# Kernel tuning notes

Hardware: AMD Instinct MI355X
Metric: run time of the kernel (lower is better)

## Reference

```python
import jax, jax.numpy as jnp
import numpy as np

N, F, E, LIN, C, B = 16384, 500, 128, 128, 10, 4096
P_EDGE = 0.002  # ~32 avg degree


def _l2norm(x):
    # F.normalize(dim=1), eps=1e-12
    n = jnp.linalg.norm(x, axis=1, keepdims=True)
    return x / jnp.maximum(n, 1e-12)


def setup_inputs() -> dict:
    key = jax.random.key(0)
    ks = jax.random.split(key, 10)
    adj = (jax.random.uniform(ks[0], (N, N)) < P_EDGE).astype(jnp.float32)
    idx = jnp.arange(N)
    adj = adj.at[idx, idx].set(1.0)  # self-loops guarantee degree >= 1
    data = jax.random.normal(ks[1], (N, F), dtype=jnp.float32)
    nodes = jax.random.randint(ks[2], (B,), 0, N)
    # Encoder 1: Linear(2F -> E); Encoder 2: Linear(2E -> E); classifier heads
    W1 = jax.random.normal(ks[3], (E, 2 * F), dtype=jnp.float32) * 0.03
    b1 = jnp.zeros((E,), jnp.float32)
    W2 = jax.random.normal(ks[4], (E, 2 * E), dtype=jnp.float32) * 0.06
    b2 = jnp.zeros((E,), jnp.float32)
    Wl1 = jax.random.normal(ks[5], (LIN, E), dtype=jnp.float32) * 0.08
    bl1 = jnp.zeros((LIN,), jnp.float32)
    Wl2 = jax.random.normal(ks[6], (C, LIN), dtype=jnp.float32) * 0.12
    bl2 = jnp.zeros((C,), jnp.float32)
    return {"nodes": nodes, "adj": adj, "data": data,
            "W1": W1, "b1": b1, "W2": W2, "b2": b2,
            "Wl1": Wl1, "bl1": bl1, "Wl2": Wl2, "bl2": bl2}


def reference(nodes, adj, data, W1, b1, W2, b2, Wl1, bl1, Wl2, bl2):
    deg = jnp.sum(adj, axis=1, keepdims=True)  # [N,1]
    # Layer 1 (mean aggregator over full neighbor set): computed for all nodes
    neigh1 = (adj @ data) / deg                               # [N,F]
    h1 = jnp.concatenate([data, neigh1], axis=1)              # [N,2F] (self, neigh)
    H1 = _l2norm(jax.nn.relu(h1 @ W1.T + b1))                 # [N,E]
    # Layer 2: only for the queried node batch
    neigh2 = (adj[nodes] @ H1) / deg[nodes]                   # [B,E]
    h2 = jnp.concatenate([H1[nodes], neigh2], axis=1)         # [B,2E]
    H2 = _l2norm(jax.nn.relu(h2 @ W2.T + b2))                 # [B,E]
    x = H2 @ Wl1.T + bl1                                      # [B,LIN]
    x = x @ Wl2.T + bl2                                       # [B,C]
    return jax.nn.softmax(x, axis=1)
```

## Files before the change

### kernel.cpp

```cpp
#include <hip/hip_runtime.h>
#include <math.h>
#include <stddef.h>

#define N_NODES 16384
#define F_DIM   500
#define KP1     512
#define E_DIM   128
#define C_DIM   10
#define B_DIM   4096
#define MAXDEG  128

typedef __attribute__((ext_vector_type(8))) short short8;
typedef __attribute__((ext_vector_type(4))) float f32x4;

__device__ inline unsigned short f2bf(float f) {
    union { float f; unsigned int u; } v; v.f = f;
    unsigned int u = v.u;
    u += 0x7FFFu + ((u >> 16) & 1u);
    return (unsigned short)(u >> 16);
}

__global__ __launch_bounds__(256) void k_prep_w1b(const float* __restrict__ W1,
                                                  unsigned short* __restrict__ Wt) {
    int idx = blockIdx.x * 256 + threadIdx.x;
    int n = idx >> 9, k = idx & 511;
    float v = (k < F_DIM) ? W1[(size_t)(n & 127) * 1000 + (n >> 7) * F_DIM + k] : 0.0f;
    Wt[idx] = f2bf(v);
}

__global__ __launch_bounds__(256) void k_prep_w2b(const float* __restrict__ W2,
                                                  unsigned short* __restrict__ Wt) {
    int idx = blockIdx.x * 256 + threadIdx.x;
    int n = idx >> 7, k = idx & 127;
    Wt[idx] = f2bf(W2[(size_t)(n & 127) * 256 + (n >> 7) * 128 + k]);
}

__global__ void k_tp(const float* __restrict__ src, float* __restrict__ dst) {
    __shared__ float tile[32][33];
    const int k0 = blockIdx.x * 32;
    const int e0 = blockIdx.y * 32;
    const int tx = threadIdx.x, ty0 = threadIdx.y;
#pragma unroll
    for (int q = 0; q < 4; ++q) {
        int ty = ty0 + q * 8;
        tile[ty][tx] = src[(size_t)(e0 + ty) * 128 + k0 + tx];
    }
    __syncthreads();
#pragma unroll
    for (int q = 0; q < 4; ++q) {
        int ty = ty0 + q * 8;
        dst[(size_t)(k0 + ty) * 128 + e0 + tx] = tile[tx][ty];
    }
}

__global__ __launch_bounds__(256) void k_gemm_mfma(const void* __restrict__ Ap,
                                                   int Ka, int Kpad, int a_fp32,
                                                   const unsigned short* __restrict__ B,
                                                   float* __restrict__ Cout) {
    __shared__ unsigned short sA[32 * 40];
    __shared__ unsigned short sB[256 * 40];
    const int tid  = threadIdx.x;
    const int w    = tid >> 6;
    const int lane = tid & 63;
    const int l16  = lane & 15;
    const int quad = lane >> 4;
    const int blockM = blockIdx.x * 32;
    f32x4 acc[2][4] = {};
    const int nchunks = Kpad >> 5;

    for (int c = 0; c < nchunks; ++c) {
        const int k0 = c << 5;
        if (tid < 128) {
            int row = tid >> 2, cc = tid & 3;
            int kbase = k0 + cc * 8;
            short8 v;
            if (a_fp32) {
                const float* Arow = (const float*)Ap + (size_t)(blockM + row) * Ka;
                float4 f0 = (kbase + 4 <= Ka) ? *(const float4*)(Arow + kbase)
                                              : make_float4(0.f, 0.f, 0.f, 0.f);
                float4 f1 = (kbase + 8 <= Ka) ? *(const float4*)(Arow + kbase + 4)
                                              : make_float4(0.f, 0.f, 0.f, 0.f);
                v[0] = (short)f2bf(f0.x); v[1] = (short)f2bf(f0.y);
                v[2] = (short)f2bf(f0.z); v[3] = (short)f2bf(f0.w);
                v[4] = (short)f2bf(f1.x); v[5] = (short)f2bf(f1.y);
                v[6] = (short)f2bf(f1.z); v[7] = (short)f2bf(f1.w);
            } else {
                v = *(const short8*)((const unsigned short*)Ap +
                                     (size_t)(blockM + row) * Ka + kbase);
            }
            *(short8*)(sA + row * 40 + cc * 8) = v;
        }
#pragma unroll
        for (int q = 0; q < 4; ++q) {
            int idx = tid + 256 * q;
            int row = idx >> 2, cc = idx & 3;
            short8 v = *(const short8*)(B + (size_t)row * Kpad + k0 + cc * 8);
            *(short8*)(sB + row * 40 + cc * 8) = v;
        }
        __syncthreads();
        short8 af[2], bf[4];
#pragma unroll
        for (int mt = 0; mt < 2; ++mt)
            af[mt] = *(const short8*)(sA + (mt * 16 + l16) * 40 + quad * 8);
#pragma unroll
        for (int nt = 0; nt < 4; ++nt)
            bf[nt] = *(const short8*)(sB + (w * 64 + nt * 16 + l16) * 40 + quad * 8);
#pragma unroll
        for (int mt = 0; mt < 2; ++mt)
#pragma unroll
            for (int nt = 0; nt < 4; ++nt)
                acc[mt][nt] = __builtin_amdgcn_mfma_f32_16x16x32_bf16(af[mt], bf[nt], acc[mt][nt], 0, 0, 0);
        __syncthreads();
    }
#pragma unroll
    for (int mt = 0; mt < 2; ++mt)
#pragma unroll
        for (int nt = 0; nt < 4; ++nt) {
            int col = w * 64 + nt * 16 + l16;
#pragma unroll
            for (int r = 0; r < 4; ++r) {
                int row = blockM + mt * 16 + quad * 4 + r;
                Cout[(size_t)row * 256 + col] = acc[mt][nt][r];
            }
        }
}

__global__ __launch_bounds__(256) void k_agg1(const float* __restrict__ adj,
                                              const float* __restrict__ X,
                                              const float* __restrict__ b1,
                                              unsigned short* __restrict__ H1b,
                                              int* __restrict__ nbr,
                                              int* __restrict__ deg) {
    const int i = blockIdx.x;
    const int t = threadIdx.x;
    const float4* row4 = (const float4*)(adj + (size_t)i * N_NODES);
    __shared__ int s_cnt;
    __shared__ int s_idx[MAXDEG];
    __shared__ float s_part[8][128];
    __shared__ float s_w[2];
    if (t == 0) s_cnt = 0;
    __syncthreads();
    float4 v[16];
#pragma unroll
    for (int p = 0; p < 16; ++p) v[p] = row4[p * 256 + t];
#pragma unroll
    for (int p = 0; p < 16; ++p) {
        int col = p * 1024 + t * 4;
        if (v[p].x != 0.f) { int q = atomicAdd(&s_cnt, 1); if (q < MAXDEG) s_idx[q] = col;     }
        if (v[p].y != 0.f) { int q = atomicAdd(&s_cnt, 1); if (q < MAXDEG) s_idx[q] = col + 1; }
        if (v[p].z != 0.f) { int q = atomicAdd(&s_cnt, 1); if (q < MAXDEG) s_idx[q] = col + 2; }
        if (v[p].w != 0.f) { int q = atomicAdd(&s_cnt, 1); if (q < MAXDEG) s_idx[q] = col + 3; }
    }
    __syncthreads();
    int cnt = s_cnt; if (cnt > MAXDEG) cnt = MAXDEG;
    if (t < cnt) nbr[(size_t)i * MAXDEG + t] = s_idx[t];
    if (t == 0) deg[i] = cnt;
    const float inv = 1.0f / (float)cnt;
    const int g = t >> 5, l = t & 31;
    float4 a4 = make_float4(0.f, 0.f, 0.f, 0.f);
    for (int k = g; k < cnt; k += 8) {
        float4 x4 = ((const float4*)(X + (size_t)s_idx[k] * 256 + 128))[l];
        a4.x += x4.x; a4.y += x4.y; a4.z += x4.z; a4.w += x4.w;
    }
    *(float4*)&s_part[g][l * 4] = a4;
    __syncthreads();
    float vv = 0.f;
    if (t < 128) {
        float tot = 0.f;
#pragma unroll
        for (int g2 = 0; g2 < 8; ++g2) tot += s_part[g2][t];
        vv = X[(size_t)i * 256 + t] + tot * inv + b1[t];
        vv = fmaxf(vv, 0.f);
        float s = vv * vv;
#pragma unroll
        for (int off = 32; off > 0; off >>= 1) s += __shfl_down(s, off, 64);
        if ((t & 63) == 0) s_w[t >> 6] = s;
    }
    __syncthreads();
    if (t < 128) {
        float denom = fmaxf(sqrtf(s_w[0] + s_w[1]), 1e-12f);
        H1b[(size_t)i * 128 + t] = f2bf(vv / denom);
    }
}

__global__ __launch_bounds__(256) void k_l2head(const int* __restrict__ nodes,
                                                const int* __restrict__ nbr,
                                                const int* __restrict__ deg,
                                                const float* __restrict__ Y,
                                                const float* __restrict__ b2,
                                                const float* __restrict__ Wl1t,
                                                const float* __restrict__ bl1,
                                                const float* __restrict__ Wl2,
                                                const float* __restrict__ bl2,
                                                float* __restrict__ out) {
    const int b = blockIdx.x;
    const int t = threadIdx.x;
    const int n = nodes[b];
    const int cnt = deg[n];
    __shared__ int s_idx[MAXDEG];
    __shared__ float s_part[8][128];
    __shared__ float s_h[128];
    __shared__ float s_x[128];
    __shared__ float s_c[C_DIM];
    __shared__ float s_w[2];
    if (t < cnt) s_idx[t] = nbr[(size_t)n * MAXDEG + t];
    __syncthreads();
    const int g = t >> 5, l = t & 31;
    float4 a4 = make_float4(0.f, 0.f, 0.f, 0.f);
    for (int k = g; k < cnt; k += 8) {
        float4 y4 = ((const float4*)(Y + (size_t)s_idx[k] * 256 + 128))[l];
        a4.x += y4.x; a4.y += y4.y; a4.z += y4.z; a4.w += y4.w;
    }
    *(float4*)&s_part[g][l * 4] = a4;
    __syncthreads();
    if (t < 128) {
        float tot = 0.f;
#pragma unroll
        for (int g2 = 0; g2 < 8; ++g2) tot += s_part[g2][t];
        float vv = Y[(size_t)n * 256 + t] + tot / (float)cnt + b2[t];
        vv = fmaxf(vv, 0.f);
        float s = vv * vv;
#pragma unroll
        for (int off = 32; off > 0; off >>= 1) s += __shfl_down(s, off, 64);
        if ((t & 63) == 0) s_w[t >> 6] = s;
        __syncthreads();
        float denom = fmaxf(sqrtf(s_w[0] + s_w[1]), 1e-12f);
        s_h[t] = vv / denom;
    } else {
        __syncthreads();
    }
    __syncthreads();
    if (t < 128) {
        float x1 = bl1[t];
#pragma unroll 8
        for (int kk = 0; kk < 128; ++kk)
            x1 += Wl1t[kk * 128 + t] * s_h[kk];
        s_x[t] = x1;
    }
    __syncthreads();
    if (t < C_DIM) {
        float l2 = bl2[t];
        const float* wr = Wl2 + (size_t)t * 128;
        for (int kk = 0; kk < 128; ++kk) l2 += wr[kk] * s_x[kk];
        s_c[t] = l2;
    }
    __syncthreads();
    if (t < C_DIM) {
        float mx = -1e30f;
        for (int c = 0; c < C_DIM; ++c) mx = fmaxf(mx, s_c[c]);
        float se = 0.f;
        for (int c = 0; c < C_DIM; ++c) se += expf(s_c[c] - mx);
        out[(size_t)b * C_DIM + t] = expf(s_c[t] - mx) / se;
    }
}

extern "C" void kernel_launch(void* const* d_in, const int* in_sizes, int n_in,
                              void* d_out, int out_size, void* d_ws, size_t ws_size,
                              hipStream_t stream) {
    const int*   nodes = (const int*)  d_in[0];
    const float* adj   = (const float*)d_in[1];
    const float* data  = (const float*)d_in[2];
    const float* W1    = (const float*)d_in[3];
    const float* b1    = (const float*)d_in[4];
    const float* W2    = (const float*)d_in[5];
    const float* b2    = (const float*)d_in[6];
    const float* Wl1   = (const float*)d_in[7];
    const float* bl1   = (const float*)d_in[8];
    const float* Wl2   = (const float*)d_in[9];
    const float* bl2   = (const float*)d_in[10];
    float* out = (float*)d_out;

    unsigned short* Wt1 = (unsigned short*)d_ws;
    unsigned short* Wt2 = Wt1 + 256 * KP1;
    unsigned short* H1b = Wt2 + 256 * 128;
    float* Wl1t = (float*)(H1b + (size_t)N_NODES * 128);
    float* X    = Wl1t + 128 * 128;
    float* Y    = X    + (size_t)N_NODES * 256;
    int*   nbr  = (int*)(Y + (size_t)N_NODES * 256);
    int*   deg  = nbr + (size_t)N_NODES * MAXDEG;

    k_prep_w1b <<<512, 256, 0, stream>>>(W1, Wt1);
    k_prep_w2b <<<128, 256, 0, stream>>>(W2, Wt2);
    k_tp<<<dim3(4, 4), dim3(32, 8), 0, stream>>>(Wl1, Wl1t);

    k_gemm_mfma<<<N_NODES / 32, 256, 0, stream>>>(data, F_DIM, KP1, 1, Wt1, X);
    k_agg1     <<<N_NODES, 256, 0, stream>>>(adj, X, b1, H1b, nbr, deg);

    k_gemm_mfma<<<N_NODES / 32, 256, 0, stream>>>(H1b, E_DIM, E_DIM, 0, Wt2, Y);
    k_l2head   <<<B_DIM, 256, 0, stream>>>(nodes, nbr, deg, Y, b2, Wl1t, bl1, Wl2, bl2, out);
}
```

Baseline: 1.424 ms.

## Overlap layer-1 GEMM with adjacency scan in one mixed kernel, split gather

```diff
diff --git a/kernel.cpp b/kernel.cpp
--- a/kernel.cpp
+++ b/kernel.cpp
@@ -20,41 +20,179 @@
     return (unsigned short)(u >> 16);
 }
 
-__global__ __launch_bounds__(256) void k_prep_w1b(const float* __restrict__ W1,
-                                                  unsigned short* __restrict__ Wt) {
-    int idx = blockIdx.x * 256 + threadIdx.x;
-    int n = idx >> 9, k = idx & 511;
-    float v = (k < F_DIM) ? W1[(size_t)(n & 127) * 1000 + (n >> 7) * F_DIM + k] : 0.0f;
-    Wt[idx] = f2bf(v);
-}
-
-__global__ __launch_bounds__(256) void k_prep_w2b(const float* __restrict__ W2,
-                                                  unsigned short* __restrict__ Wt) {
-    int idx = blockIdx.x * 256 + threadIdx.x;
-    int n = idx >> 7, k = idx & 127;
-    Wt[idx] = f2bf(W2[(size_t)(n & 127) * 256 + (n >> 7) * 128 + k]);
-}
-
-__global__ void k_tp(const float* __restrict__ src, float* __restrict__ dst) {
-    __shared__ float tile[32][33];
-    const int k0 = blockIdx.x * 32;
-    const int e0 = blockIdx.y * 32;
-    const int tx = threadIdx.x, ty0 = threadIdx.y;
-#pragma unroll
-    for (int q = 0; q < 4; ++q) {
-        int ty = ty0 + q * 8;
-        tile[ty][tx] = src[(size_t)(e0 + ty) * 128 + k0 + tx];
-    }
-    __syncthreads();
-#pragma unroll
-    for (int q = 0; q < 4; ++q) {
-        int ty = ty0 + q * 8;
-        dst[(size_t)(k0 + ty) * 128 + e0 + tx] = tile[tx][ty];
-    }
-}
-
-__global__ __launch_bounds__(256) void k_gemm_mfma(const void* __restrict__ Ap,
-                                                   int Ka, int Kpad, int a_fp32,
+__global__ __launch_bounds__(256) void k_prep(const float* __restrict__ W1,
+                                              const float* __restrict__ W2,
+                                              const float* __restrict__ Wl1,
+                                              unsigned short* __restrict__ Wt1,
+                                              unsigned short* __restrict__ Wt2,
+                                              float* __restrict__ Wl1t) {
+    const int bb = blockIdx.x;
+    const int t = threadIdx.x;
+    if (bb < 512) {
+        int idx = bb * 256 + t;
+        int n = idx >> 9, k = idx & 511;
+        float v = (k < F_DIM) ? W1[(size_t)(n & 127) * 1000 + (n >> 7) * F_DIM + k] : 0.0f;
+        Wt1[idx] = f2bf(v);
+    } else if (bb < 640) {
+        int idx = (bb - 512) * 256 + t;
+        int n = idx >> 7, k = idx & 127;
+        Wt2[idx] = f2bf(W2[(size_t)(n & 127) * 256 + (n >> 7) * 128 + k]);
+    } else {
+        __shared__ float tile[32][33];
+        int tb = bb - 640;
+        int k0 = (tb & 3) * 32, e0 = (tb >> 2) * 32;
+        int tx = t & 31, ty0 = t >> 5;
+#pragma unroll
+        for (int q = 0; q < 4; ++q) {
+            int ty = ty0 + q * 8;
+            tile[ty][tx] = Wl1[(size_t)(e0 + ty) * 128 + k0 + tx];
+        }
+        __syncthreads();
+#pragma unroll
+        for (int q = 0; q < 4; ++q) {
+            int ty = ty0 + q * 8;
+            Wl1t[(size_t)(k0 + ty) * 128 + e0 + tx] = tile[tx][ty];
+        }
+    }
+}
+
+__global__ __launch_bounds__(256) void k_mix(const float* __restrict__ data,
+                                             const unsigned short* __restrict__ Wt1,
+                                             float* __restrict__ X,
+                                             const float* __restrict__ adj,
+                                             unsigned short* __restrict__ nbr,
+                                             int* __restrict__ deg) {
+    __shared__ alignas(16) unsigned char s_raw[(32 * 40 + 256 * 40) * 2];
+    const int bb = blockIdx.x;
+    const int tid = threadIdx.x;
+
+    if (bb < 512) {
+        unsigned short* sA = (unsigned short*)s_raw;
+        unsigned short* sB = sA + 32 * 40;
+        const int w    = tid >> 6;
+        const int lane = tid & 63;
+        const int l16  = lane & 15;
+        const int quad = lane >> 4;
+        const int blockM = bb * 32;
+        f32x4 acc[2][4] = {};
+#pragma unroll 1
+        for (int c = 0; c < (KP1 >> 5); ++c) {
+            const int k0 = c << 5;
+            if (tid < 128) {
+                int row = tid >> 2, cc = tid & 3;
+                int kbase = k0 + cc * 8;
+                const float* Arow = data + (size_t)(blockM + row) * F_DIM;
+                float4 f0 = (kbase + 4 <= F_DIM) ? *(const float4*)(Arow + kbase)
+                                                 : make_float4(0.f, 0.f, 0.f, 0.f);
+                float4 f1 = (kbase + 8 <= F_DIM) ? *(const float4*)(Arow + kbase + 4)
+                                                 : make_float4(0.f, 0.f, 0.f, 0.f);
+                short8 v;
+                v[0] = (short)f2bf(f0.x); v[1] = (short)f2bf(f0.y);
+                v[2] = (short)f2bf(f0.z); v[3] = (short)f2bf(f0.w);
+                v[4] = (short)f2bf(f1.x); v[5] = (short)f2bf(f1.y);
+                v[6] = (short)f2bf(f1.z); v[7] = (short)f2bf(f1.w);
+                *(short8*)(sA + row * 40 + cc * 8) = v;
+            }
+#pragma unroll
+            for (int q = 0; q < 4; ++q) {
+                int idx = tid + 256 * q;
+                int row = idx >> 2, cc = idx & 3;
+                short8 v = *(const short8*)(Wt1 + (size_t)row * KP1 + k0 + cc * 8);
+                *(short8*)(sB + row * 40 + cc * 8) = v;
+            }
+            __syncthreads();
+            short8 af[2], bf[4];
+#pragma unroll
+            for (int mt = 0; mt < 2; ++mt)
+                af[mt] = *(const short8*)(sA + (mt * 16 + l16) * 40 + quad * 8);
+#pragma unroll
+            for (int nt = 0; nt < 4; ++nt)
+                bf[nt] = *(const short8*)(sB + (w * 64 + nt * 16 + l16) * 40 + quad * 8);
+#pragma unroll
+            for (int mt = 0; mt < 2; ++mt)
+#pragma unroll
+                for (int nt = 0; nt < 4; ++nt)
+                    acc[mt][nt] = __builtin_amdgcn_mfma_f32_16x16x32_bf16(af[mt], bf[nt], acc[mt][nt], 0, 0, 0);
+            __syncthreads();
+        }
+#pragma unroll
+        for (int mt = 0; mt < 2; ++mt)
+#pragma unroll
+            for (int nt = 0; nt < 4; ++nt) {
+                int col = w * 64 + nt * 16 + l16;
+#pragma unroll
+                for (int r = 0; r < 4; ++r) {
+                    int row = blockM + mt * 16 + quad * 4 + r;
+                    X[(size_t)row * 256 + col] = acc[mt][nt][r];
+                }
+            }
+    } else {
+        const int i = bb - 512;
+        int* s_cnt = (int*)s_raw;
+        int* s_idx = ((int*)s_raw) + 4;
+        const float4* row4 = (const float4*)(adj + (size_t)i * N_NODES);
+        if (tid == 0) *s_cnt = 0;
+        __syncthreads();
+        float4 v[16];
+#pragma unroll
+        for (int p = 0; p < 16; ++p) v[p] = row4[p * 256 + tid];
+#pragma unroll
+        for (int p = 0; p < 16; ++p) {
+            int col = p * 1024 + tid * 4;
+            if (v[p].x != 0.f) { int q = atomicAdd(s_cnt, 1); if (q < MAXDEG) s_idx[q] = col;     }
+            if (v[p].y != 0.f) { int q = atomicAdd(s_cnt, 1); if (q < MAXDEG) s_idx[q] = col + 1; }
+            if (v[p].z != 0.f) { int q = atomicAdd(s_cnt, 1); if (q < MAXDEG) s_idx[q] = col + 2; }
+            if (v[p].w != 0.f) { int q = atomicAdd(s_cnt, 1); if (q < MAXDEG) s_idx[q] = col + 3; }
+        }
+        __syncthreads();
+        int cnt = *s_cnt; if (cnt > MAXDEG) cnt = MAXDEG;
+        if (tid < cnt) nbr[(size_t)i * MAXDEG + tid] = (unsigned short)s_idx[tid];
+        if (tid == 0) deg[i] = cnt;
+    }
+}
+
+__global__ __launch_bounds__(256) void k_gather(const unsigned short* __restrict__ nbr,
+                                                const int* __restrict__ deg,
+                                                const float* __restrict__ X,
+                                                const float* __restrict__ b1,
+                                                unsigned short* __restrict__ H1b) {
+    const int i = blockIdx.x;
+    const int t = threadIdx.x;
+    const int cnt = deg[i];
+    __shared__ int s_idx[MAXDEG];
+    __shared__ float s_part[8][128];
+    __shared__ float s_w[2];
+    if (t < cnt) s_idx[t] = nbr[(size_t)i * MAXDEG + t];
+    __syncthreads();
+    const int g = t >> 5, l = t & 31;
+    float4 a4 = make_float4(0.f, 0.f, 0.f, 0.f);
+    for (int k = g; k < cnt; k += 8) {
+        float4 x4 = ((const float4*)(X + (size_t)s_idx[k] * 256 + 128))[l];
+        a4.x += x4.x; a4.y += x4.y; a4.z += x4.z; a4.w += x4.w;
+    }
+    *(float4*)&s_part[g][l * 4] = a4;
+    __syncthreads();
+    float vv = 0.f;
+    if (t < 128) {
+        float tot = 0.f;
+#pragma unroll
+        for (int g2 = 0; g2 < 8; ++g2) tot += s_part[g2][t];
+        vv = X[(size_t)i * 256 + t] + tot / (float)cnt + b1[t];
+        vv = fmaxf(vv, 0.f);
+        float s = vv * vv;
+#pragma unroll
+        for (int off = 32; off > 0; off >>= 1) s += __shfl_down(s, off, 64);
+        if ((t & 63) == 0) s_w[t >> 6] = s;
+    }
+    __syncthreads();
+    if (t < 128) {
+        float denom = fmaxf(sqrtf(s_w[0] + s_w[1]), 1e-12f);
+        H1b[(size_t)i * 128 + t] = f2bf(vv / denom);
+    }
+}
+
+__global__ __launch_bounds__(256) void k_gemm_mfma(const unsigned short* __restrict__ A,
+                                                   int K,
                                                    const unsigned short* __restrict__ B,
                                                    float* __restrict__ Cout) {
     __shared__ unsigned short sA[32 * 40];
@@ -66,35 +204,18 @@
     const int quad = lane >> 4;
     const int blockM = blockIdx.x * 32;
     f32x4 acc[2][4] = {};
-    const int nchunks = Kpad >> 5;
-
-    for (int c = 0; c < nchunks; ++c) {
+    for (int c = 0; c < (K >> 5); ++c) {
         const int k0 = c << 5;
         if (tid < 128) {
             int row = tid >> 2, cc = tid & 3;
-            int kbase = k0 + cc * 8;
-            short8 v;
-            if (a_fp32) {
-                const float* Arow = (const float*)Ap + (size_t)(blockM + row) * Ka;
-                float4 f0 = (kbase + 4 <= Ka) ? *(const float4*)(Arow + kbase)
-                                              : make_float4(0.f, 0.f, 0.f, 0.f);
-                float4 f1 = (kbase + 8 <= Ka) ? *(const float4*)(Arow + kbase + 4)
-                                              : make_float4(0.f, 0.f, 0.f, 0.f);
-                v[0] = (short)f2bf(f0.x); v[1] = (short)f2bf(f0.y);
-                v[2] = (short)f2bf(f0.z); v[3] = (short)f2bf(f0.w);
-                v[4] = (short)f2bf(f1.x); v[5] = (short)f2bf(f1.y);
-                v[6] = (short)f2bf(f1.z); v[7] = (short)f2bf(f1.w);
-            } else {
-                v = *(const short8*)((const unsigned short*)Ap +
-                                     (size_t)(blockM + row) * Ka + kbase);
-            }
+            short8 v = *(const short8*)(A + (size_t)(blockM + row) * K + k0 + cc * 8);
             *(short8*)(sA + row * 40 + cc * 8) = v;
         }
 #pragma unroll
         for (int q = 0; q < 4; ++q) {
             int idx = tid + 256 * q;
             int row = idx >> 2, cc = idx & 3;
-            short8 v = *(const short8*)(B + (size_t)row * Kpad + k0 + cc * 8);
+            short8 v = *(const short8*)(B + (size_t)row * K + k0 + cc * 8);
             *(short8*)(sB + row * 40 + cc * 8) = v;
         }
         __syncthreads();
@@ -125,66 +246,8 @@
         }
 }
 
-__global__ __launch_bounds__(256) void k_agg1(const float* __restrict__ adj,
-                                              const float* __restrict__ X,
-                                              const float* __restrict__ b1,
-                                              unsigned short* __restrict__ H1b,
-                                              int* __restrict__ nbr,
-                                              int* __restrict__ deg) {
-    const int i = blockIdx.x;
-    const int t = threadIdx.x;
-    const float4* row4 = (const float4*)(adj + (size_t)i * N_NODES);
-    __shared__ int s_cnt;
-    __shared__ int s_idx[MAXDEG];
-    __shared__ float s_part[8][128];
-    __shared__ float s_w[2];
-    if (t == 0) s_cnt = 0;
-    __syncthreads();
-    float4 v[16];
-#pragma unroll
-    for (int p = 0; p < 16; ++p) v[p] = row4[p * 256 + t];
-#pragma unroll
-    for (int p = 0; p < 16; ++p) {
-        int col = p * 1024 + t * 4;
-        if (v[p].x != 0.f) { int q = atomicAdd(&s_cnt, 1); if (q < MAXDEG) s_idx[q] = col;     }
-        if (v[p].y != 0.f) { int q = atomicAdd(&s_cnt, 1); if (q < MAXDEG) s_idx[q] = col + 1; }
-        if (v[p].z != 0.f) { int q = atomicAdd(&s_cnt, 1); if (q < MAXDEG) s_idx[q] = col + 2; }
-        if (v[p].w != 0.f) { int q = atomicAdd(&s_cnt, 1); if (q < MAXDEG) s_idx[q] = col + 3; }
-    }
-    __syncthreads();
-    int cnt = s_cnt; if (cnt > MAXDEG) cnt = MAXDEG;
-    if (t < cnt) nbr[(size_t)i * MAXDEG + t] = s_idx[t];
-    if (t == 0) deg[i] = cnt;
-    const float inv = 1.0f / (float)cnt;
-    const int g = t >> 5, l = t & 31;
-    float4 a4 = make_float4(0.f, 0.f, 0.f, 0.f);
-    for (int k = g; k < cnt; k += 8) {
-        float4 x4 = ((const float4*)(X + (size_t)s_idx[k] * 256 + 128))[l];
-        a4.x += x4.x; a4.y += x4.y; a4.z += x4.z; a4.w += x4.w;
-    }
-    *(float4*)&s_part[g][l * 4] = a4;
-    __syncthreads();
-    float vv = 0.f;
-    if (t < 128) {
-        float tot = 0.f;
-#pragma unroll
-        for (int g2 = 0; g2 < 8; ++g2) tot += s_part[g2][t];
-        vv = X[(size_t)i * 256 + t] + tot * inv + b1[t];
-        vv = fmaxf(vv, 0.f);
-        float s = vv * vv;
-#pragma unroll
-        for (int off = 32; off > 0; off >>= 1) s += __shfl_down(s, off, 64);
-        if ((t & 63) == 0) s_w[t >> 6] = s;
-    }
-    __syncthreads();
-    if (t < 128) {
-        float denom = fmaxf(sqrtf(s_w[0] + s_w[1]), 1e-12f);
-        H1b[(size_t)i * 128 + t] = f2bf(vv / denom);
-    }
-}
-
 __global__ __launch_bounds__(256) void k_l2head(const int* __restrict__ nodes,
-                                                const int* __restrict__ nbr,
+                                                const unsigned short* __restrict__ nbr,
                                                 const int* __restrict__ deg,
                                                 const float* __restrict__ Y,
                                                 const float* __restrict__ b2,
@@ -276,16 +339,14 @@
     float* Wl1t = (float*)(H1b + (size_t)N_NODES * 128);
     float* X    = Wl1t + 128 * 128;
     float* Y    = X    + (size_t)N_NODES * 256;
-    int*   nbr  = (int*)(Y + (size_t)N_NODES * 256);
-    int*   deg  = nbr + (size_t)N_NODES * MAXDEG;
-
-    k_prep_w1b <<<512, 256, 0, stream>>>(W1, Wt1);
-    k_prep_w2b <<<128, 256, 0, stream>>>(W2, Wt2);
-    k_tp<<<dim3(4, 4), dim3(32, 8), 0, stream>>>(Wl1, Wl1t);
-
-    k_gemm_mfma<<<N_NODES / 32, 256, 0, stream>>>(data, F_DIM, KP1, 1, Wt1, X);
-    k_agg1     <<<N_NODES, 256, 0, stream>>>(adj, X, b1, H1b, nbr, deg);
-
-    k_gemm_mfma<<<N_NODES / 32, 256, 0, stream>>>(H1b, E_DIM, E_DIM, 0, Wt2, Y);
+    unsigned short* nbr = (unsigned short*)(Y + (size_t)N_NODES * 256);
+    int*   deg  = (int*)(nbr + (size_t)N_NODES * MAXDEG);
+
+    k_prep<<<656, 256, 0, stream>>>(W1, W2, Wl1, Wt1, Wt2, Wl1t);
+
+    k_mix   <<<512 + N_NODES, 256, 0, stream>>>(data, Wt1, X, adj, nbr, deg);
+    k_gather<<<N_NODES, 256, 0, stream>>>(nbr, deg, X, b1, H1b);
+
+    k_gemm_mfma<<<N_NODES / 32, 256, 0, stream>>>(H1b, E_DIM, Wt2, Y);
     k_l2head   <<<B_DIM, 256, 0, stream>>>(nodes, nbr, deg, Y, b2, Wl1t, bl1, Wl2, bl2, out);
 }
```

New measurement: 1.423 ms. Within noise of the previous version (-0.1%).
